# Optimization experiments

Measured on AMD Instinct MI355X. Metric: run time of the kernel, lower is better.

The kernel has to match this reference:

```python
import jax, jax.numpy as jnp
import numpy as np

D_IN = 1024
D_OUT = 1024
N, S = 4, 2048

def setup_inputs() -> dict:
    key = jax.random.key(0)
    kv, kk, kq, k1, k2, k3 = jax.random.split(key, 6)
    return {
        "v": jax.random.normal(kv, (N, S, D_IN), dtype=jnp.float32),
        "k": jax.random.normal(kk, (N, S, D_IN), dtype=jnp.float32),
        "q": jax.random.normal(kq, (N, S, D_IN), dtype=jnp.float32),
        "WV": jax.random.normal(k1, (D_OUT, D_IN), dtype=jnp.float32),
        "WQ": jax.random.normal(k2, (D_OUT, D_IN), dtype=jnp.float32),
        "WK": jax.random.normal(k3, (D_OUT, D_IN), dtype=jnp.float32),
    }

def reference(v, k, q, WV, WQ, WK) -> jnp.ndarray:
    # projections: x @ W.T  -> [N, S, D_OUT]
    wv = jnp.einsum('nsw,ow->nso', v, WV)
    wk = jnp.einsum('nsw,ow->nso', k, WK)
    wq = jnp.einsum('nsw,ow->nso', q, WQ)
    # scores [N, Sq, Sk]; NOTE: softmax over axis=1 (query axis, matching torch dim=1),
    # then post-hoc division by input_shape[0] AFTER softmax (faithful to source).
    scores = jnp.einsum('nqo,nko->nqk', wq, wk)
    wqk = jax.nn.softmax(scores, axis=1) / jnp.float32(D_IN)
    return jnp.einsum('nqk,nko->nqo', wqk, wv)
```

## Files before the change

### kernel.cpp

```cpp
#include <hip/hip_runtime.h>
#include <math.h>


typedef _Float16 f16;
typedef _Float16 f16x8 __attribute__((ext_vector_type(8)));
typedef _Float16 f16x4 __attribute__((ext_vector_type(4)));
typedef float f32x4 __attribute__((ext_vector_type(4)));

enum StageMode { SM_PLANES2, SM_PLANES1 };
enum EpiMode   { EPI_F32, EPI_SPLIT, EPI_F16T };

#define GLL_PITCH 32

__device__ __forceinline__ void gll16(const f16* g, f16* l) {
    __builtin_amdgcn_global_load_lds(
        (const __attribute__((address_space(1))) void*)g,
        (__attribute__((address_space(3))) void*)l, 16, 0, 0);
}

__device__ __forceinline__ void stage_gll_plane(const f16* __restrict__ gplane,
                                                f16* __restrict__ lds,
                                                long rowBase, int ld, int k0,
                                                int wave, int lane)
{
#pragma unroll
    for (int i = 0; i < 2; i++) {
        int slotBase = (wave * 2 + i) * 64;
        int t = slotBase + lane;
        int r = t >> 2;
        int c = (t & 3) ^ ((r >> 1) & 3);
        const f16* g = gplane + (rowBase + r) * (long)ld + k0 + c * 8;
        gll16(g, lds + (long)slotBase * 8);
    }
}

__device__ __forceinline__ int frag_off_gll(int row, int g) {
    return row * GLL_PITCH + ((g ^ ((row >> 1) & 3)) << 3);
}

template<StageMode SA, StageMode SB, EpiMode EP, int GROUPM, bool STATS>
__global__ __launch_bounds__(256, 4)
void mfma_gemm(const f16* __restrict__ Ahi, const f16* __restrict__ Alo,
               const f16* __restrict__ Bhi, const f16* __restrict__ Blo,
               float* __restrict__ pmOut, float* __restrict__ psOut,
               void* __restrict__ C0, void* __restrict__ C1,
               int M, int Nc, int K, int lda, int ldb, int ldc,
               long batchA, long batchB, long batchC,
               float epiScale, int tsShift)
{
    constexpr bool TRIPLE = (SA == SM_PLANES2);
    constexpr int PLANE_SZ = 128 * GLL_PITCH;

    int bx, by;
    if constexpr (GROUPM > 0) {
        int gx = gridDim.x;
        int lin = blockIdx.y * gx + blockIdx.x;
        int nig = GROUPM * gx;
        int gid = lin / nig;
        int rem = lin - gid * nig;
        by = gid * GROUPM + (rem % GROUPM);
        bx = rem / GROUPM;
    } else {
        bx = blockIdx.x;
        by = blockIdx.y;
    }
    const int n0 = bx * 128;
    const int m0 = by * 128;
    const long z = blockIdx.z;

    const long aOfs = z * batchA, bOfs = z * batchB, cOfs = z * batchC;

    __shared__ __align__(16) f16 As_hi[PLANE_SZ];
    __shared__ __align__(16) f16 Bs_hi[PLANE_SZ];
    __shared__ __align__(16) f16 As_lo[TRIPLE ? PLANE_SZ : 8];
    __shared__ __align__(16) f16 Bs_lo[TRIPLE ? PLANE_SZ : 8];

    const int tid  = threadIdx.x;
    const int lane = tid & 63;
    const int wave = tid >> 6;
    const int wr = (wave >> 1) * 64;
    const int wc = (wave & 1) * 64;
    const int fm = lane & 15;
    const int fg = lane >> 4;

    f32x4 acc[4][4];
#pragma unroll
    for (int i = 0; i < 4; i++)
#pragma unroll
        for (int j = 0; j < 4; j++) acc[i][j] = (f32x4){0.f, 0.f, 0.f, 0.f};

    int roA[4], roB[4];
#pragma unroll
    for (int i = 0; i < 4; i++) {
        roA[i] = frag_off_gll(wr + i * 16 + fm, fg);
        roB[i] = frag_off_gll(wc + i * 16 + fm, fg);
    }

    for (int k0 = 0; k0 < K; k0 += 32) {
        stage_gll_plane(Ahi + aOfs, As_hi, m0, lda, k0, wave, lane);
        stage_gll_plane(Bhi + bOfs, Bs_hi, n0, ldb, k0, wave, lane);
        if constexpr (TRIPLE) {
            stage_gll_plane(Alo + aOfs, As_lo, m0, lda, k0, wave, lane);
            stage_gll_plane(Blo + bOfs, Bs_lo, n0, ldb, k0, wave, lane);
        }
        __syncthreads();

        f16x8 ah[4], bh[4], al[4], bl[4];
#pragma unroll
        for (int i = 0; i < 4; i++) {
            ah[i] = *(const f16x8*)&As_hi[roA[i]];
            bh[i] = *(const f16x8*)&Bs_hi[roB[i]];
            if constexpr (TRIPLE) {
                al[i] = *(const f16x8*)&As_lo[roA[i]];
                bl[i] = *(const f16x8*)&Bs_lo[roB[i]];
            }
        }
#pragma unroll
        for (int i = 0; i < 4; i++) {
#pragma unroll
            for (int j = 0; j < 4; j++) {
                acc[i][j] = __builtin_amdgcn_mfma_f32_16x16x32_f16(ah[i], bh[j], acc[i][j], 0, 0, 0);
                if constexpr (TRIPLE) {
                    acc[i][j] = __builtin_amdgcn_mfma_f32_16x16x32_f16(ah[i], bl[j], acc[i][j], 0, 0, 0);
                    acc[i][j] = __builtin_amdgcn_mfma_f32_16x16x32_f16(al[i], bh[j], acc[i][j], 0, 0, 0);
                }
            }
        }
        __syncthreads();
    }

    const int cr = fg * 4;
    const int cn = fm;
#pragma unroll
    for (int i = 0; i < 4; i++) {
#pragma unroll
        for (int j = 0; j < 4; j++) {
#pragma unroll
            for (int r = 0; r < 4; r++) {
                long mg = m0 + wr + i * 16 + cr + r;
                long ng = n0 + wc + j * 16 + cn;
                float val = acc[i][j][r] * epiScale;
                if constexpr (EP == EPI_F32) {
                    ((float*)C0)[cOfs + mg * ldc + ng] = val;
                } else if constexpr (EP == EPI_SPLIT) {
                    f16 h = (f16)val;
                    ((f16*)C0)[cOfs + mg * ldc + ng] = h;
                    ((f16*)C1)[cOfs + mg * ldc + ng] = (f16)(val - (float)h);
                } else {
                    long TS = 1L << tsShift;
                    long nb = mg >> tsShift;
                    long s  = mg & (TS - 1);
                    long addr = nb * ((long)Nc << tsShift) + ng * TS + s;
                    ((f16*)C0)[addr] = (f16)val;
                }
            }
        }
    }
}

template<EpiMode EP, bool STATS, int XCDMODE, bool DUAL, bool TRIPLE>
__global__ __launch_bounds__(512, 2)
void big_gemm(const f16* __restrict__ Ahi, const f16* __restrict__ Alo,
              const f16* __restrict__ Bhi, const f16* __restrict__ Blo,
              const f16* __restrict__ A2hi, const f16* __restrict__ A2lo,
              const f16* __restrict__ B2hi, const f16* __restrict__ B2lo,
              float* __restrict__ pmOut, float* __restrict__ psOut,
              void* __restrict__ C0, void* __restrict__ C1,
              void* __restrict__ C20, void* __restrict__ C21,
              int M, int Nc, int K, int lda, int ldb, int ldc,
              long batchA, long batchB, long batchC, int msplitTiles)
{
    constexpr int PLANE = 256 * GLL_PITCH;

    __shared__ __align__(16) f16 As_hi[2][PLANE];
    __shared__ __align__(16) f16 Bs_hi[2][PLANE];
    __shared__ __align__(16) f16 As_lo[2][TRIPLE ? PLANE : 8];
    __shared__ __align__(16) f16 Bs_lo[2][TRIPLE ? PLANE : 8];

    const int tid  = threadIdx.x;
    const int lane = tid & 63;
    const int wave = tid >> 6;
    const int rw   = wave >> 2;
    const int cw   = wave & 3;
    const int wrM  = rw * 128;
    const int wrN  = cw * 64;
    const int fm   = lane & 15;
    const int fg   = lane >> 4;

    int bxn, byn, zn;
    if constexpr (XCDMODE == 1) {
        const int Lid = (int)(blockIdx.z * 64 + blockIdx.y * 8 + blockIdx.x);
        const int xcd = Lid & 7;
        const int sct = Lid >> 3;
        bxn = sct & 7;
        const int idxp = xcd * 4 + (sct >> 3);
        byn = idxp & 7;
        zn  = idxp >> 3;
    } else if constexpr (XCDMODE == 2) {
        const int Lid = (int)(blockIdx.y * 4 + blockIdx.x);
        const int xcd = Lid & 7;
        const int sct = Lid >> 3;
        bxn = sct & 3;
        byn = xcd * 8 + (sct >> 2);
        zn  = 0;
    } else {
        bxn = blockIdx.x;
        byn = blockIdx.y;
        zn  = blockIdx.z;
    }

    const f16* pAhi = Ahi; const f16* pAlo = Alo;
    const f16* pBhi = Bhi; const f16* pBlo = Blo;
    void* pC0 = C0; void* pC1 = C1;
    int mTile = byn;
    if constexpr (DUAL) {
        if (byn >= msplitTiles) {
            pAhi = A2hi; pAlo = A2lo; pBhi = B2hi; pBlo = B2lo;
            pC0 = C20; pC1 = C21;
            mTile = byn - msplitTiles;
        }
    }

    const int n0 = bxn * 256;
    const int m0 = mTile * 256;
    const long z = zn;
    const long aOfs = z * batchA, bOfs = z * batchB, cOfs = z * batchC;

    int slotBase[2], srcA[2], srcB[2];
#pragma unroll
    for (int i = 0; i < 2; i++) {
        int sb = (wave * 2 + i) * 64;
        int t  = sb + lane;
        int r  = t >> 2;
        int c  = (t & 3) ^ ((r >> 1) & 3);
        slotBase[i] = sb * 8;
        srcA[i] = (m0 + r) * lda + c * 8;
        srcB[i] = (n0 + r) * ldb + c * 8;
    }

#define SC_STAGE(buf, k0) do {                                                   \
    _Pragma("unroll")                                                            \
    for (int s_ = 0; s_ < 2; s_++) {                                             \
        gll16(pAhi + aOfs + srcA[s_] + (k0), &As_hi[buf][slotBase[s_]]);         \
        gll16(pBhi + bOfs + srcB[s_] + (k0), &Bs_hi[buf][slotBase[s_]]);         \
        if constexpr (TRIPLE) {                                                  \
            gll16(pAlo + aOfs + srcA[s_] + (k0), &As_lo[buf][slotBase[s_]]);     \
            gll16(pBlo + bOfs + srcB[s_] + (k0), &Bs_lo[buf][slotBase[s_]]);     \
        }                                                                        \
    } } while (0)

    f32x4 acc[8][4];
#pragma unroll
    for (int i = 0; i < 8; i++)
#pragma unroll
        for (int j = 0; j < 4; j++) acc[i][j] = (f32x4){0.f, 0.f, 0.f, 0.f};

    int roA[8], roB[4];
#pragma unroll
    for (int i = 0; i < 8; i++) roA[i] = frag_off_gll(wrM + i * 16 + fm, fg);
#pragma unroll
    for (int j = 0; j < 4; j++) roB[j] = frag_off_gll(wrN + j * 16 + fm, fg);

    const int NT = K >> 5;
    SC_STAGE(0, 0);
    SC_STAGE(1, 32);

    for (int t = 0; t < NT; t++) {
        const int cur = t & 1;
        if (t == 0) {
            if constexpr (TRIPLE) asm volatile("s_waitcnt vmcnt(8)" ::: "memory");
            else                  asm volatile("s_waitcnt vmcnt(4)" ::: "memory");
        } else {
            asm volatile("s_waitcnt vmcnt(0)" ::: "memory");
        }
        __builtin_amdgcn_sched_barrier(0);
        __builtin_amdgcn_s_barrier();
        __builtin_amdgcn_sched_barrier(0);

        if (t >= 1 && t + 1 < NT) SC_STAGE(cur ^ 1, (t + 1) * 32);
        __builtin_amdgcn_sched_barrier(0);

        f16x8 bh[4], a0h[4];
#pragma unroll
        for (int j = 0; j < 4; j++) bh[j] = *(const f16x8*)&Bs_hi[cur][roB[j]];
#pragma unroll
        for (int i = 0; i < 4; i++) a0h[i] = *(const f16x8*)&As_hi[cur][roA[i]];
        __builtin_amdgcn_sched_barrier(0);
        f16x8 bl[4], a0l[4];
        if constexpr (TRIPLE) {
#pragma unroll
            for (int j = 0; j < 4; j++) bl[j] = *(const f16x8*)&Bs_lo[cur][roB[j]];
#pragma unroll
            for (int i = 0; i < 4; i++) a0l[i] = *(const f16x8*)&As_lo[cur][roA[i]];
            __builtin_amdgcn_sched_barrier(0);
        }

        __builtin_amdgcn_s_setprio(1);
#pragma unroll
        for (int i = 0; i < 4; i++)
#pragma unroll
            for (int j = 0; j < 4; j++)
                acc[i][j] = __builtin_amdgcn_mfma_f32_16x16x32_f16(a0h[i], bh[j], acc[i][j], 0, 0, 0);
        __builtin_amdgcn_s_setprio(0);
        __builtin_amdgcn_sched_barrier(0);

        f16x8 a1h[4], a1l[4];
#pragma unroll
        for (int i = 0; i < 4; i++) {
            a1h[i] = *(const f16x8*)&As_hi[cur][roA[4 + i]];
            if constexpr (TRIPLE) a1l[i] = *(const f16x8*)&As_lo[cur][roA[4 + i]];
        }
        __builtin_amdgcn_sched_barrier(0);

        if constexpr (TRIPLE) {
            __builtin_amdgcn_s_setprio(1);
#pragma unroll
            for (int i = 0; i < 4; i++)
#pragma unroll
                for (int j = 0; j < 4; j++)
                    acc[i][j] = __builtin_amdgcn_mfma_f32_16x16x32_f16(a0h[i], bl[j], acc[i][j], 0, 0, 0);
#pragma unroll
            for (int i = 0; i < 4; i++)
#pragma unroll
                for (int j = 0; j < 4; j++)
                    acc[i][j] = __builtin_amdgcn_mfma_f32_16x16x32_f16(a0l[i], bh[j], acc[i][j], 0, 0, 0);
            __builtin_amdgcn_s_setprio(0);
            __builtin_amdgcn_sched_barrier(0);
        }

        __builtin_amdgcn_s_setprio(1);
#pragma unroll
        for (int i = 0; i < 4; i++)
#pragma unroll
            for (int j = 0; j < 4; j++)
                acc[4 + i][j] = __builtin_amdgcn_mfma_f32_16x16x32_f16(a1h[i], bh[j], acc[4 + i][j], 0, 0, 0);
        if constexpr (TRIPLE) {
#pragma unroll
            for (int i = 0; i < 4; i++)
#pragma unroll
                for (int j = 0; j < 4; j++)
                    acc[4 + i][j] = __builtin_amdgcn_mfma_f32_16x16x32_f16(a1h[i], bl[j], acc[4 + i][j], 0, 0, 0);
#pragma unroll
            for (int i = 0; i < 4; i++)
#pragma unroll
                for (int j = 0; j < 4; j++)
                    acc[4 + i][j] = __builtin_amdgcn_mfma_f32_16x16x32_f16(a1l[i], bh[j], acc[4 + i][j], 0, 0, 0);
        }
        __builtin_amdgcn_s_setprio(0);
    }
#undef SC_STAGE

    const int cr = fg * 4;

    if constexpr (STATS) {
        __shared__ float stM[2][256];
        __shared__ float stS[2][256];
#pragma unroll
        for (int j = 0; j < 4; j++) {
            float mj = -3.402823466e38f;
#pragma unroll
            for (int i = 0; i < 8; i++)
#pragma unroll
                for (int r = 0; r < 4; r++) mj = fmaxf(mj, acc[i][j][r]);
            float sj = 0.f;
#pragma unroll
            for (int i = 0; i < 8; i++)
#pragma unroll
                for (int r = 0; r < 4; r++) sj += __expf(acc[i][j][r] - mj);
#pragma unroll
            for (int mask = 16; mask <= 32; mask <<= 1) {
                float mo = __shfl_xor(mj, mask, 64);
                float so = __shfl_xor(sj, mask, 64);
                float mn = fmaxf(mj, mo);
                sj = sj * __expf(mj - mn) + so * __expf(mo - mn);
                mj = mn;
            }
            if (fg == 0) {
                stM[rw][wrN + j * 16 + fm] = mj;
                stS[rw][wrN + j * 16 + fm] = sj;
            }
        }
        __syncthreads();
        if (tid < 256) {
            float ma = stM[0][tid], mb = stM[1][tid];
            float Mc = fmaxf(ma, mb);
            float Sv = stS[0][tid] * __expf(ma - Mc) + stS[1][tid] * __expf(mb - Mc);
            long o = ((long)z * (M >> 8) + byn) * (long)Nc + (long)bxn * 256 + tid;
            pmOut[o] = Mc;
            psOut[o] = Sv;
            stM[0][tid] = Mc;
        }
        __syncthreads();

#pragma unroll
        for (int j = 0; j < 4; j++) {
            const float Mc = stM[0][wrN + j * 16 + fm];
#pragma unroll
            for (int i = 0; i < 8; i++) {
#pragma unroll
                for (int r = 0; r < 4; r++) {
                    long mg = m0 + wrM + i * 16 + cr + r;
                    long ng = n0 + wrN + j * 16 + fm;
                    ((f16*)pC0)[cOfs + mg * (long)ldc + ng] =
                        (f16)__expf(acc[i][j][r] - Mc);
                }
            }
        }
    } else {
#pragma unroll
        for (int i = 0; i < 8; i++) {
#pragma unroll
            for (int j = 0; j < 4; j++) {
#pragma unroll
                for (int r = 0; r < 4; r++) {
                    long mg = m0 + wrM + i * 16 + cr + r;
                    long ng = n0 + wrN + j * 16 + fm;
                    float val = acc[i][j][r];
                    if constexpr (EP == EPI_F32) {
                        ((float*)pC0)[cOfs + mg * (long)ldc + ng] = val;
                    } else {
                        f16 h = (f16)val;
                        ((f16*)pC0)[cOfs + mg * (long)ldc + ng] = h;
                        ((f16*)pC1)[cOfs + mg * (long)ldc + ng] = (f16)(val - (float)h);
                    }
                }
            }
        }
    }
}

__global__ __launch_bounds__(256)
void split_all_kernel(const float* __restrict__ q, const float* __restrict__ k,
                      const float* __restrict__ v, const float* __restrict__ WQ,
                      const float* __restrict__ WK, const float* __restrict__ WV,
                      f16* __restrict__ ws, long NSD, long DD)
{
    const long QB = NSD / 2048;
    const long WB = DD / 2048;
    const long b = blockIdx.x;
    f16* Wb = ws + 5 * NSD;

    const float* src;
    f16* hi;
    f16* lo = nullptr;
    long base;
    if (b < QB)               { src = q;  base = b * 2048;                 hi = ws;           lo = ws + NSD;   }
    else if (b < 2 * QB)      { src = k;  base = (b - QB) * 2048;          hi = ws + 2 * NSD; lo = ws + 3 * NSD; }
    else if (b < 3 * QB)      { src = v;  base = (b - 2 * QB) * 2048;      hi = ws + 4 * NSD; }
    else if (b < 3 * QB + WB) { src = WQ; base = (b - 3 * QB) * 2048;      hi = Wb;           lo = Wb + DD;    }
    else if (b < 3 * QB + 2 * WB) { src = WK; base = (b - 3 * QB - WB) * 2048; hi = Wb + 2 * DD; lo = Wb + 3 * DD; }
    else                      { src = WV; base = (b - 3 * QB - 2 * WB) * 2048; hi = Wb + 4 * DD; }

    long i = base + (long)threadIdx.x * 8;
    float4 x0 = *(const float4*)&src[i];
    float4 x1 = *(const float4*)&src[i + 4];
    float xs[8] = {x0.x, x0.y, x0.z, x0.w, x1.x, x1.y, x1.z, x1.w};
    f16x8 h, l;
#pragma unroll
    for (int e = 0; e < 8; e++) {
        f16 hh = (f16)xs[e];
        h[e] = hh;
        l[e] = (f16)(xs[e] - (float)hh);
    }
    *(f16x8*)&hi[i] = h;
    if (lo) *(f16x8*)&lo[i] = l;
}

__global__ __launch_bounds__(256)
void pmat_kernel(f16* __restrict__ P, const float* __restrict__ pm,
                 const float* __restrict__ ps, int S)
{
    const int n = blockIdx.z;
    const int kk = blockIdx.x * 1024 + threadIdx.x * 4;
    const int q0 = blockIdx.y * 32;
    const int tile = q0 >> 8;
    f16* Pn = P + (long)n * S * S;

    float w4[4];
#pragma unroll
    for (int c = 0; c < 4; c++) {
        const int col = kk + c;
        float pmv[8];
        float M = -INFINITY;
#pragma unroll
        for (int i = 0; i < 8; i++) {
            pmv[i] = pm[((long)n * 8 + i) * S + col];
            M = fmaxf(M, pmv[i]);
        }
        float Ssum = 0.f;
#pragma unroll
        for (int i = 0; i < 8; i++)
            Ssum += ps[((long)n * 8 + i) * S + col] * __expf(pmv[i] - M);
        w4[c] = __expf(pmv[tile] - M) / Ssum;
    }

    for (int qi = 0; qi < 32; qi++) {
        long idx = (long)(q0 + qi) * S + kk;
        f16x4 ph = *(const f16x4*)&Pn[idx];
        f16x4 p;
#pragma unroll
        for (int e = 0; e < 4; e++) p[e] = (f16)((float)ph[e] * w4[e]);
        *(f16x4*)&Pn[idx] = p;
    }
}

extern "C" void kernel_launch(void* const* d_in, const int* in_sizes, int n_in,
                              void* d_out, int out_size, void* d_ws, size_t ws_size,
                              hipStream_t stream)
{
    const float* v  = (const float*)d_in[0];
    const float* k  = (const float*)d_in[1];
    const float* q  = (const float*)d_in[2];
    const float* WV = (const float*)d_in[3];
    const float* WQ = (const float*)d_in[4];
    const float* WK = (const float*)d_in[5];
    float* out = (float*)d_out;

    const int N = 4, S = 2048, D = 1024;
    const long NSD = (long)N * S * D;
    const long DD  = (long)D * D;

    f16* ws = (f16*)d_ws;
    f16* q_hi = ws;
    f16* q_lo = ws + NSD;
    f16* k_hi = ws + 2 * NSD;
    f16* k_lo = ws + 3 * NSD;
    f16* v_hi = ws + 4 * NSD;
    f16* Wb   = ws + 5 * NSD;
    f16* WQ_hi = Wb,          *WQ_lo = Wb + DD;
    f16* WK_hi = Wb + 2 * DD, *WK_lo = Wb + 3 * DD;
    f16* WV_hi = Wb + 4 * DD;
    f16* wq_hi = ws + 5 * NSD + 5 * DD;
    f16* wq_lo = wq_hi + NSD;
    f16* wk_hi = wq_hi + 2 * NSD;
    f16* wk_lo = wq_hi + 3 * NSD;
    f16* wvT_hi = ws;
    f16* Sc16   = ws + NSD;
    float* pm    = (float*)(ws + 9 * NSD + 5 * DD);
    float* ps    = pm + (long)N * 8 * S;

    dim3 blk(256);

    {
        long nblocks = 3 * (NSD / 2048) + 3 * (DD / 2048);
        split_all_kernel<<<dim3((unsigned)nblocks), blk, 0, stream>>>(
            q, k, v, WQ, WK, WV, ws, NSD, DD);
    }

    {
        dim3 g(D / 256, (2 * N * S) / 256, 1);
        big_gemm<EPI_SPLIT, false, 2, true, true><<<g, dim3(512), 0, stream>>>(
            q_hi, q_lo, WQ_hi, WQ_lo,
            k_hi, k_lo, WK_hi, WK_lo,
            nullptr, nullptr,
            wq_hi, wq_lo, wk_hi, wk_lo,
            2 * N * S, D, D, D, D, D, 0, 0, 0, (N * S) / 256 );
    }
    {
        dim3 g(D / 128, (N * S) / 128, 1);
        mfma_gemm<SM_PLANES1, SM_PLANES1, EPI_F16T, 4, false><<<g, blk, 0, stream>>>(
            v_hi, nullptr, WV_hi, nullptr, nullptr, nullptr, wvT_hi, nullptr,
            N * S, D, D, D, D, 0, 0, 0, 0, 1.0f, 11 );
    }
    {
        dim3 g(S / 256, S / 256, N);
        big_gemm<EPI_F32, true, 1, false, true><<<g, dim3(512), 0, stream>>>(
            wq_hi, wq_lo, wk_hi, wk_lo,
            nullptr, nullptr, nullptr, nullptr,
            pm, ps, Sc16, nullptr, nullptr, nullptr,
            S, S, D, D, D, S, (long)S * D, (long)S * D, (long)S * S, 1 << 30);
    }
    {
        dim3 g(S / 1024, S / 32, N);
        pmat_kernel<<<g, blk, 0, stream>>>(Sc16, pm, ps, S);
    }
    {
        dim3 g(D / 128, S / 128, N);
        mfma_gemm<SM_PLANES1, SM_PLANES1, EPI_F32, 4, false><<<g, blk, 0, stream>>>(
            Sc16, nullptr, wvT_hi, nullptr, nullptr, nullptr, out, nullptr,
            S, D, S, S, S, D, (long)S * S, (long)S * D, (long)S * D, 1.0f / (float)D, 0);
    }
}
```

Before: 444.1 us.

## Restructure GEMM main loop into multi-phase ping-pong with split hi/lo staging

Reworks the double-buffered K loop so each iteration issues the next tile's hi-plane loads right after reading the current fragments and the lo-plane loads later, with several workgroup barriers separating LDS-read and MFMA phases. The aim is to spread global-to-LDS traffic across the iteration and interleave waves' memory and MFMA phases, hiding load latency better. In exchange it adds several extra s_barriers per iteration and tighter vmcnt waits, which may cost synchronization overhead and reduce scheduler freedom.

```diff
diff --git a/kernel.cpp b/kernel.cpp
--- a/kernel.cpp
+++ b/kernel.cpp
@@ -238,16 +238,20 @@
         srcB[i] = (n0 + r) * ldb + c * 8;
     }
 
-#define SC_STAGE(buf, k0) do {                                                   \
+#define STG_HI(buf, k0) do {                                                     \
     _Pragma("unroll")                                                            \
     for (int s_ = 0; s_ < 2; s_++) {                                             \
         gll16(pAhi + aOfs + srcA[s_] + (k0), &As_hi[buf][slotBase[s_]]);         \
         gll16(pBhi + bOfs + srcB[s_] + (k0), &Bs_hi[buf][slotBase[s_]]);         \
-        if constexpr (TRIPLE) {                                                  \
-            gll16(pAlo + aOfs + srcA[s_] + (k0), &As_lo[buf][slotBase[s_]]);     \
-            gll16(pBlo + bOfs + srcB[s_] + (k0), &Bs_lo[buf][slotBase[s_]]);     \
-        }                                                                        \
     } } while (0)
+#define STG_LO(buf, k0) do {                                                     \
+    _Pragma("unroll")                                                            \
+    for (int s_ = 0; s_ < 2; s_++) {                                             \
+        gll16(pAlo + aOfs + srcA[s_] + (k0), &As_lo[buf][slotBase[s_]]);         \
+        gll16(pBlo + bOfs + srcB[s_] + (k0), &Bs_lo[buf][slotBase[s_]]);         \
+    } } while (0)
+#define SBAR() do { __builtin_amdgcn_sched_barrier(0);                           \
+    __builtin_amdgcn_s_barrier(); __builtin_amdgcn_sched_barrier(0); } while (0)
 
     f32x4 acc[8][4];
 #pragma unroll
@@ -262,39 +266,28 @@
     for (int j = 0; j < 4; j++) roB[j] = frag_off_gll(wrN + j * 16 + fm, fg);
 
     const int NT = K >> 5;
-    SC_STAGE(0, 0);
-    SC_STAGE(1, 32);
+
+    STG_HI(0, 0);
+    if constexpr (TRIPLE) {
+        STG_LO(0, 0);
+        asm volatile("s_waitcnt vmcnt(4)" ::: "memory");
+    } else {
+        asm volatile("s_waitcnt vmcnt(0)" ::: "memory");
+    }
+    SBAR();
 
     for (int t = 0; t < NT; t++) {
         const int cur = t & 1;
-        if (t == 0) {
-            if constexpr (TRIPLE) asm volatile("s_waitcnt vmcnt(8)" ::: "memory");
-            else                  asm volatile("s_waitcnt vmcnt(4)" ::: "memory");
-        } else {
-            asm volatile("s_waitcnt vmcnt(0)" ::: "memory");
-        }
-        __builtin_amdgcn_sched_barrier(0);
-        __builtin_amdgcn_s_barrier();
-        __builtin_amdgcn_sched_barrier(0);
-
-        if (t >= 1 && t + 1 < NT) SC_STAGE(cur ^ 1, (t + 1) * 32);
-        __builtin_amdgcn_sched_barrier(0);
+        const bool more = (t + 1 < NT);
+        const int kN = (t + 1) * 32;
 
         f16x8 bh[4], a0h[4];
 #pragma unroll
         for (int j = 0; j < 4; j++) bh[j] = *(const f16x8*)&Bs_hi[cur][roB[j]];
 #pragma unroll
         for (int i = 0; i < 4; i++) a0h[i] = *(const f16x8*)&As_hi[cur][roA[i]];
-        __builtin_amdgcn_sched_barrier(0);
-        f16x8 bl[4], a0l[4];
-        if constexpr (TRIPLE) {
-#pragma unroll
-            for (int j = 0; j < 4; j++) bl[j] = *(const f16x8*)&Bs_lo[cur][roB[j]];
-#pragma unroll
-            for (int i = 0; i < 4; i++) a0l[i] = *(const f16x8*)&As_lo[cur][roA[i]];
-            __builtin_amdgcn_sched_barrier(0);
-        }
-
+        if (more) STG_HI(cur ^ 1, kN);
+        SBAR();
         __builtin_amdgcn_s_setprio(1);
 #pragma unroll
         for (int i = 0; i < 4; i++)
@@ -302,39 +295,51 @@
             for (int j = 0; j < 4; j++)
                 acc[i][j] = __builtin_amdgcn_mfma_f32_16x16x32_f16(a0h[i], bh[j], acc[i][j], 0, 0, 0);
         __builtin_amdgcn_s_setprio(0);
-        __builtin_amdgcn_sched_barrier(0);
-
-        f16x8 a1h[4], a1l[4];
-#pragma unroll
-        for (int i = 0; i < 4; i++) {
-            a1h[i] = *(const f16x8*)&As_hi[cur][roA[4 + i]];
-            if constexpr (TRIPLE) a1l[i] = *(const f16x8*)&As_lo[cur][roA[4 + i]];
-        }
-        __builtin_amdgcn_sched_barrier(0);
-
         if constexpr (TRIPLE) {
+            if (more) asm volatile("s_waitcnt vmcnt(4)" ::: "memory");
+            else      asm volatile("s_waitcnt vmcnt(0)" ::: "memory");
+        }
+        SBAR();
+
+        if constexpr (TRIPLE) {
+            f16x8 bl[4], a0l[4];
+#pragma unroll
+            for (int j = 0; j < 4; j++) bl[j] = *(const f16x8*)&Bs_lo[cur][roB[j]];
+#pragma unroll
+            for (int i = 0; i < 4; i++) a0l[i] = *(const f16x8*)&As_lo[cur][roA[i]];
+            if (more) STG_LO(cur ^ 1, kN);
+            SBAR();
             __builtin_amdgcn_s_setprio(1);
 #pragma unroll
             for (int i = 0; i < 4; i++)
 #pragma unroll
                 for (int j = 0; j < 4; j++)
                     acc[i][j] = __builtin_amdgcn_mfma_f32_16x16x32_f16(a0h[i], bl[j], acc[i][j], 0, 0, 0);
+            __builtin_amdgcn_s_setprio(0);
+            SBAR();
+
+            f16x8 a1h[4], a1l[4];
+#pragma unroll
+            for (int i = 0; i < 4; i++) {
+                a1h[i] = *(const f16x8*)&As_hi[cur][roA[4 + i]];
+                a1l[i] = *(const f16x8*)&As_lo[cur][roA[4 + i]];
+            }
+            SBAR();
+            __builtin_amdgcn_s_setprio(1);
 #pragma unroll
             for (int i = 0; i < 4; i++)
 #pragma unroll
                 for (int j = 0; j < 4; j++)
                     acc[i][j] = __builtin_amdgcn_mfma_f32_16x16x32_f16(a0l[i], bh[j], acc[i][j], 0, 0, 0);
             __builtin_amdgcn_s_setprio(0);
-            __builtin_amdgcn_sched_barrier(0);
-        }
-
-        __builtin_amdgcn_s_setprio(1);
-#pragma unroll
-        for (int i = 0; i < 4; i++)
-#pragma unroll
-            for (int j = 0; j < 4; j++)
-                acc[4 + i][j] = __builtin_amdgcn_mfma_f32_16x16x32_f16(a1h[i], bh[j], acc[4 + i][j], 0, 0, 0);
-        if constexpr (TRIPLE) {
+            SBAR();
+
+            __builtin_amdgcn_s_setprio(1);
+#pragma unroll
+            for (int i = 0; i < 4; i++)
+#pragma unroll
+                for (int j = 0; j < 4; j++)
+                    acc[4 + i][j] = __builtin_amdgcn_mfma_f32_16x16x32_f16(a1h[i], bh[j], acc[4 + i][j], 0, 0, 0);
 #pragma unroll
             for (int i = 0; i < 4; i++)
 #pragma unroll
@@ -345,10 +350,29 @@
 #pragma unroll
                 for (int j = 0; j < 4; j++)
                     acc[4 + i][j] = __builtin_amdgcn_mfma_f32_16x16x32_f16(a1l[i], bh[j], acc[4 + i][j], 0, 0, 0);
-        }
-        __builtin_amdgcn_s_setprio(0);
-    }
-#undef SC_STAGE
+            __builtin_amdgcn_s_setprio(0);
+            if (more) asm volatile("s_waitcnt vmcnt(4)" ::: "memory");
+            else      asm volatile("s_waitcnt vmcnt(0)" ::: "memory");
+            SBAR();
+        } else {
+            f16x8 a1h[4];
+#pragma unroll
+            for (int i = 0; i < 4; i++) a1h[i] = *(const f16x8*)&As_hi[cur][roA[4 + i]];
+            SBAR();
+            __builtin_amdgcn_s_setprio(1);
+#pragma unroll
+            for (int i = 0; i < 4; i++)
+#pragma unroll
+                for (int j = 0; j < 4; j++)
+                    acc[4 + i][j] = __builtin_amdgcn_mfma_f32_16x16x32_f16(a1h[i], bh[j], acc[4 + i][j], 0, 0, 0);
+            __builtin_amdgcn_s_setprio(0);
+            asm volatile("s_waitcnt vmcnt(0)" ::: "memory");
+            SBAR();
+        }
+    }
+#undef STG_HI
+#undef STG_LO
+#undef SBAR
 
     const int cr = fg * 4;
 
```

Result: no change. 442.5 us (-0.3%).
